# Kernel tuning notes

Measured on AMD Instinct MI355X. Metric: run time of the kernel, lower is better.

The kernel has to match this reference:

```python
import jax, jax.numpy as jnp
import numpy as np

B, C, H, WID = 32, 64, 128, 128
K = 5            # co-occurrence bins (co_shape)
WH = 3           # spatial filter height/width (w_shape = (1,3,3), depth 1)
ACT_LO, ACT_HI = 0.0, 1.0  # actBounds


def setup_inputs() -> dict:
    key = jax.random.key(0)
    k1, k2, k3 = jax.random.split(key, 3)
    input_tensor = jax.random.uniform(k1, (B, C, H, WID), dtype=jnp.float32)
    # learned params: L ~ N(0, 0.1) of shape (k,k); W ~ N(0,0.1) of shape (d,h,w)
    L = 0.1 * jax.random.normal(k2, (K, K), dtype=jnp.float32)
    W = 0.1 * jax.random.normal(k3, (1, WH, WH), dtype=jnp.float32)
    return {"input_tensor": input_tensor, "W": W, "L": L}


def _quantize(x, k):
    # map activation in [ACT_LO, ACT_HI] to bin index in [0, k-1]
    b = jnp.floor((x - ACT_LO) / (ACT_HI - ACT_LO) * k)
    return jnp.clip(b, 0, k - 1).astype(jnp.int32)


def reference(input_tensor, W, L):
    """Co-occurrence layer:
    out[p] = sum_{q in 3x3 nbhd(p)} W[q-p] * L[bin(x[q]), bin(x[p])] * x[q]
    Out-of-bounds neighbors contribute 0 (zero pad => x[q]=0 kills the term),
    matching the precomputed neighbor_lookup_table boundary handling.
    """
    k = L.shape[0]
    pad = WH // 2
    bins = _quantize(input_tensor, k)                      # (B,C,H,W) int32
    xp = jnp.pad(input_tensor, ((0, 0), (0, 0), (pad, pad), (pad, pad)))
    bp = jnp.pad(bins, ((0, 0), (0, 0), (pad, pad), (pad, pad)))
    h, w = input_tensor.shape[2], input_tensor.shape[3]
    out = jnp.zeros_like(input_tensor)
    for dh in range(WH):                                   # tiny fixed 3x3 loop
        for dw in range(WH):
            xn = xp[:, :, dh:dh + h, dw:dw + w]            # shifted neighbor values
            bn = bp[:, :, dh:dh + h, dw:dw + w]            # shifted neighbor bins
            out = out + W[0, dh, dw] * L[bn, bins] * xn    # gather L + weighted acc
    return out
```

## Files before the change

kernel.cpp:

```cpp
#include <hip/hip_runtime.h>


namespace {
constexpr int H  = 128;
constexpr int WD = 128;
constexpr int PLANES = 32 * 64;
constexpr int PX = 8;
constexpr int RPT = 2;
constexpr int ROWS_PER_BLOCK = 32;
constexpr int THREADS = (ROWS_PER_BLOCK / RPT) * (WD / PX);
constexpr int TILES = H / ROWS_PER_BLOCK;

typedef float vfloat4 __attribute__((ext_vector_type(4)));
}

__global__ __launch_bounds__(THREADS, 4) void col_kernel(
    const float* __restrict__ x, const float* __restrict__ Wf,
    const float* __restrict__ Lf, float* __restrict__ out)
{
    __shared__ float WL[9 * 25];
    const int t = threadIdx.x;
    if (t < 225) WL[t] = Wf[t / 25] * Lf[t % 25];
    __syncthreads();

    const int plane = blockIdx.x >> 2;
    const int tile  = blockIdx.x & 3;
    const int row0  = tile * ROWS_PER_BLOCK + (t >> 4) * RPT;
    const int col0  = (t & 15) * PX;

    const float* xp = x + (size_t)plane * (H * WD);

    float win[4][PX + 2];
    #pragma unroll
    for (int k = 0; k < 4; ++k) {
        const int rr = row0 + k - 1;
        const bool vr = (rr >= 0) && (rr < H);
        const float* rp = xp + rr * WD + col0;
        float4 c0 = make_float4(0.f, 0.f, 0.f, 0.f);
        float4 c1 = make_float4(0.f, 0.f, 0.f, 0.f);
        float l = 0.f, r = 0.f;
        if (vr) {
            c0 = *(const float4*)rp;
            c1 = *(const float4*)(rp + 4);
            if (col0 > 0)       l = rp[-1];
            if (col0 < WD - PX) r = rp[PX];
        }
        win[k][0] = l;
        win[k][1] = c0.x; win[k][2] = c0.y; win[k][3] = c0.z; win[k][4] = c0.w;
        win[k][5] = c1.x; win[k][6] = c1.y; win[k][7] = c1.z; win[k][8] = c1.w;
        win[k][9] = r;
    }

    int bq20[4][PX + 2];
    int bp4a[PX], bp4b[PX];
    #pragma unroll
    for (int k = 0; k < 4; ++k) {
        #pragma unroll
        for (int j = 0; j < PX + 2; ++j) {
            int b = (int)(win[k][j] * 5.0f);
            b = (b > 4) ? 4 : b;
            bq20[k][j] = b * 20;
            if (k == 1 && j >= 1 && j <= PX) bp4a[j - 1] = b * 4;
            if (k == 2 && j >= 1 && j <= PX) bp4b[j - 1] = b * 4;
        }
    }

    const char* wlb = (const char*)WL;
    float acca[PX], accb[PX];
    #pragma unroll
    for (int i = 0; i < PX; ++i) { acca[i] = 0.f; accb[i] = 0.f; }

    #pragma unroll
    for (int dr = 0; dr < 3; ++dr) {
        #pragma unroll
        for (int dw = 0; dw < 3; ++dw) {
            const int imm = (dr * 3 + dw) * 100;
            float lwa[PX], lwb[PX];
            #pragma unroll
            for (int i = 0; i < PX; ++i)
                lwa[i] = *(const float*)(wlb + (bq20[dr][i + dw] + bp4a[i] + imm));
            #pragma unroll
            for (int i = 0; i < PX; ++i)
                lwb[i] = *(const float*)(wlb + (bq20[dr + 1][i + dw] + bp4b[i] + imm));
            #pragma unroll
            for (int i = 0; i < PX; ++i)
                acca[i] = fmaf(lwa[i], win[dr][i + dw], acca[i]);
            #pragma unroll
            for (int i = 0; i < PX; ++i)
                accb[i] = fmaf(lwb[i], win[dr + 1][i + dw], accb[i]);
        }
    }

    float* op = out + (size_t)plane * (H * WD) + row0 * WD + col0;
    vfloat4 sa0 = { acca[0], acca[1], acca[2], acca[3] };
    vfloat4 sa1 = { acca[4], acca[5], acca[6], acca[7] };
    vfloat4 sb0 = { accb[0], accb[1], accb[2], accb[3] };
    vfloat4 sb1 = { accb[4], accb[5], accb[6], accb[7] };
    __builtin_nontemporal_store(sa0, (vfloat4*)op);
    __builtin_nontemporal_store(sa1, (vfloat4*)(op + 4));
    __builtin_nontemporal_store(sb0, (vfloat4*)(op + WD));
    __builtin_nontemporal_store(sb1, (vfloat4*)(op + WD + 4));
}

extern "C" void kernel_launch(void* const* d_in, const int* in_sizes, int n_in,
                              void* d_out, int out_size, void* d_ws, size_t ws_size,
                              hipStream_t stream) {
    const float* x  = (const float*)d_in[0];
    const float* Wf = (const float*)d_in[1];
    const float* Lf = (const float*)d_in[2];
    float* out = (float*)d_out;

    col_kernel<<<dim3(PLANES * TILES), dim3(THREADS), 0, stream>>>(x, Wf, Lf, out);
}
```

Measured before the change: 245.4 us.

## Process whole plane per block with rolling row window and prefetch

Each block now covers a full 128x128 plane, and each thread walks 8 rows in 4 steps of 2 rows using a rotating 4-row register window. The next two rows are loaded before the current step's compute. This removes the re-read of halo rows between row tiles, cuts the per-block LDS table setup by a factor of four, and overlaps global loads with the gather/FMA work. In exchange the grid has a quarter as many blocks, register pressure rises (the launch-bounds occupancy hint drops from 4 to 3), and the nontemporal stores become ordinary stores.

```diff
diff --git a/kernel.cpp b/kernel.cpp
--- a/kernel.cpp
+++ b/kernel.cpp
@@ -6,15 +6,11 @@
 constexpr int WD = 128;
 constexpr int PLANES = 32 * 64;
 constexpr int PX = 8;
-constexpr int RPT = 2;
-constexpr int ROWS_PER_BLOCK = 32;
-constexpr int THREADS = (ROWS_PER_BLOCK / RPT) * (WD / PX);
-constexpr int TILES = H / ROWS_PER_BLOCK;
-
-typedef float vfloat4 __attribute__((ext_vector_type(4)));
+constexpr int STEPS = 4;
+constexpr int THREADS = 256;
 }
 
-__global__ __launch_bounds__(THREADS, 4) void col_kernel(
+__global__ __launch_bounds__(THREADS, 3) void col_kernel(
     const float* __restrict__ x, const float* __restrict__ Wf,
     const float* __restrict__ Lf, float* __restrict__ out)
 {
@@ -23,83 +19,111 @@
     if (t < 225) WL[t] = Wf[t / 25] * Lf[t % 25];
     __syncthreads();
 
-    const int plane = blockIdx.x >> 2;
-    const int tile  = blockIdx.x & 3;
-    const int row0  = tile * ROWS_PER_BLOCK + (t >> 4) * RPT;
-    const int col0  = (t & 15) * PX;
+    const int col0 = (t & 15) * PX;
+    const int r0   = (t >> 4) * (2 * STEPS);
 
-    const float* xp = x + (size_t)plane * (H * WD);
+    const float* xp = x + (size_t)blockIdx.x * (H * WD);
+    float* opb      = out + (size_t)blockIdx.x * (H * WD);
+
+    auto load_row = [&](int rr, float v[PX + 2]) {
+        if (rr >= 0 && rr < H) {
+            const float* rp = xp + rr * WD + col0;
+            float4 c0 = *(const float4*)rp;
+            float4 c1 = *(const float4*)(rp + 4);
+            v[0] = (col0 > 0) ? rp[-1] : 0.f;
+            v[1] = c0.x; v[2] = c0.y; v[3] = c0.z; v[4] = c0.w;
+            v[5] = c1.x; v[6] = c1.y; v[7] = c1.z; v[8] = c1.w;
+            v[9] = (col0 < WD - PX) ? rp[PX] : 0.f;
+        } else {
+            #pragma unroll
+            for (int j = 0; j < PX + 2; ++j) v[j] = 0.f;
+        }
+    };
+    auto quant_row = [&](const float v[PX + 2], int bq[PX + 2]) {
+        #pragma unroll
+        for (int j = 0; j < PX + 2; ++j) {
+            int b = (int)(v[j] * 5.0f);
+            b = (b > 4) ? 4 : b;
+            bq[j] = b * 20;
+        }
+    };
 
     float win[4][PX + 2];
+    int   bq20[4][PX + 2];
     #pragma unroll
     for (int k = 0; k < 4; ++k) {
-        const int rr = row0 + k - 1;
-        const bool vr = (rr >= 0) && (rr < H);
-        const float* rp = xp + rr * WD + col0;
-        float4 c0 = make_float4(0.f, 0.f, 0.f, 0.f);
-        float4 c1 = make_float4(0.f, 0.f, 0.f, 0.f);
-        float l = 0.f, r = 0.f;
-        if (vr) {
-            c0 = *(const float4*)rp;
-            c1 = *(const float4*)(rp + 4);
-            if (col0 > 0)       l = rp[-1];
-            if (col0 < WD - PX) r = rp[PX];
-        }
-        win[k][0] = l;
-        win[k][1] = c0.x; win[k][2] = c0.y; win[k][3] = c0.z; win[k][4] = c0.w;
-        win[k][5] = c1.x; win[k][6] = c1.y; win[k][7] = c1.z; win[k][8] = c1.w;
-        win[k][9] = r;
-    }
-
-    int bq20[4][PX + 2];
-    int bp4a[PX], bp4b[PX];
-    #pragma unroll
-    for (int k = 0; k < 4; ++k) {
-        #pragma unroll
-        for (int j = 0; j < PX + 2; ++j) {
-            int b = (int)(win[k][j] * 5.0f);
-            b = (b > 4) ? 4 : b;
-            bq20[k][j] = b * 20;
-            if (k == 1 && j >= 1 && j <= PX) bp4a[j - 1] = b * 4;
-            if (k == 2 && j >= 1 && j <= PX) bp4b[j - 1] = b * 4;
-        }
+        load_row(r0 - 1 + k, win[k]);
+        quant_row(win[k], bq20[k]);
     }
 
     const char* wlb = (const char*)WL;
-    float acca[PX], accb[PX];
-    #pragma unroll
-    for (int i = 0; i < PX; ++i) { acca[i] = 0.f; accb[i] = 0.f; }
 
     #pragma unroll
-    for (int dr = 0; dr < 3; ++dr) {
+    for (int s = 0; s < STEPS; ++s) {
+        const int pa = (s & 1) ? 2 : 0;
+        const int pb = (s & 1) ? 3 : 1;
+        const int pc = (s & 1) ? 0 : 2;
+        const int pd = (s & 1) ? 1 : 3;
+        const int r  = r0 + 2 * s;
+
+        float nxt0[PX + 2], nxt1[PX + 2];
+        if (s < STEPS - 1) {
+            load_row(r + 3, nxt0);
+            load_row(r + 4, nxt1);
+        }
+
+        int bp4a[PX], bp4b[PX];
         #pragma unroll
-        for (int dw = 0; dw < 3; ++dw) {
-            const int imm = (dr * 3 + dw) * 100;
-            float lwa[PX], lwb[PX];
+        for (int i = 0; i < PX; ++i) {
+            bp4a[i] = (bq20[pb][i + 1] * 52429) >> 18;
+            bp4b[i] = (bq20[pc][i + 1] * 52429) >> 18;
+        }
+
+        float acca[PX], accb[PX];
+        #pragma unroll
+        for (int i = 0; i < PX; ++i) { acca[i] = 0.f; accb[i] = 0.f; }
+
+        const int R0[3] = {pa, pb, pc};
+        const int R1[3] = {pb, pc, pd};
+
+        #pragma unroll
+        for (int dr = 0; dr < 3; ++dr) {
             #pragma unroll
-            for (int i = 0; i < PX; ++i)
-                lwa[i] = *(const float*)(wlb + (bq20[dr][i + dw] + bp4a[i] + imm));
+            for (int dw = 0; dw < 3; ++dw) {
+                const int imm = (dr * 3 + dw) * 100;
+                float lwa[PX], lwb[PX];
+                #pragma unroll
+                for (int i = 0; i < PX; ++i)
+                    lwa[i] = *(const float*)(
+                        wlb + (bq20[R0[dr]][i + dw] + bp4a[i] + imm));
+                #pragma unroll
+                for (int i = 0; i < PX; ++i)
+                    lwb[i] = *(const float*)(
+                        wlb + (bq20[R1[dr]][i + dw] + bp4b[i] + imm));
+                #pragma unroll
+                for (int i = 0; i < PX; ++i)
+                    acca[i] = fmaf(lwa[i], win[R0[dr]][i + dw], acca[i]);
+                #pragma unroll
+                for (int i = 0; i < PX; ++i)
+                    accb[i] = fmaf(lwb[i], win[R1[dr]][i + dw], accb[i]);
+            }
+        }
+
+        float* op = opb + r * WD + col0;
+        *(float4*)op            = make_float4(acca[0], acca[1], acca[2], acca[3]);
+        *(float4*)(op + 4)      = make_float4(acca[4], acca[5], acca[6], acca[7]);
+        *(float4*)(op + WD)     = make_float4(accb[0], accb[1], accb[2], accb[3]);
+        *(float4*)(op + WD + 4) = make_float4(accb[4], accb[5], accb[6], accb[7]);
+
+        if (s < STEPS - 1) {
             #pragma unroll
-            for (int i = 0; i < PX; ++i)
-                lwb[i] = *(const float*)(wlb + (bq20[dr + 1][i + dw] + bp4b[i] + imm));
+            for (int j = 0; j < PX + 2; ++j) win[pa][j] = nxt0[j];
+            quant_row(win[pa], bq20[pa]);
             #pragma unroll
-            for (int i = 0; i < PX; ++i)
-                acca[i] = fmaf(lwa[i], win[dr][i + dw], acca[i]);
-            #pragma unroll
-            for (int i = 0; i < PX; ++i)
-                accb[i] = fmaf(lwb[i], win[dr + 1][i + dw], accb[i]);
+            for (int j = 0; j < PX + 2; ++j) win[pb][j] = nxt1[j];
+            quant_row(win[pb], bq20[pb]);
         }
     }
-
-    float* op = out + (size_t)plane * (H * WD) + row0 * WD + col0;
-    vfloat4 sa0 = { acca[0], acca[1], acca[2], acca[3] };
-    vfloat4 sa1 = { acca[4], acca[5], acca[6], acca[7] };
-    vfloat4 sb0 = { accb[0], accb[1], accb[2], accb[3] };
-    vfloat4 sb1 = { accb[4], accb[5], accb[6], accb[7] };
-    __builtin_nontemporal_store(sa0, (vfloat4*)op);
-    __builtin_nontemporal_store(sa1, (vfloat4*)(op + 4));
-    __builtin_nontemporal_store(sb0, (vfloat4*)(op + WD));
-    __builtin_nontemporal_store(sb1, (vfloat4*)(op + WD + 4));
 }
 
 extern "C" void kernel_launch(void* const* d_in, const int* in_sizes, int n_in,
@@ -110,5 +134,5 @@
     const float* Lf = (const float*)d_in[2];
     float* out = (float*)d_out;
 
-    col_kernel<<<dim3(PLANES * TILES), dim3(THREADS), 0, stream>>>(x, Wf, Lf, out);
+    col_kernel<<<dim3(PLANES), dim3(THREADS), 0, stream>>>(x, Wf, Lf, out);
 }
```

New measurement: 346.1 us. +41.1%, slower.
